# Optimization experiments

Hardware: AMD Instinct MI355X
Metric: run time of the kernel (lower is better)

## Reference

```python
import jax, jax.numpy as jnp
import numpy as np

LORA_R = 32
LORA_ALPHA = 64
SCALING = LORA_ALPHA / LORA_R  # LoraLinear.scaling_
INIT_STD = 0.02  # router_init_range_


def setup_inputs() -> dict:
    key = jax.random.key(0)
    k0, k1, k2, k3, k4 = jax.random.split(key, 5)
    B, S, D, O, E, R = 4, 4096, 3072, 3072, 8, LORA_R
    x = jax.random.normal(k0, (B, S, D), jnp.float32)
    W = jax.random.normal(k1, (O, D), jnp.float32) * INIT_STD          # base_layer weight
    gate_w = jax.random.normal(k2, (E, D), jnp.float32) * INIT_STD     # router gate
    lora_A = jax.random.normal(k3, (E, R, D), jnp.float32) * INIT_STD  # per-expert lora_A.weight
    lora_B = jax.random.normal(k4, (E, O, R), jnp.float32) * INIT_STD  # per-expert lora_B.weight
    return {"x": x, "W": W, "gate_w": gate_w, "lora_A": lora_A, "lora_B": lora_B, "top_k": 2}


def reference(x, W, gate_w, lora_A, lora_B, top_k):
    # MixLoRA routing: softmax gate -> top-k -> renormalize -> per-expert LoRA -> combine.
    B, S, D = x.shape
    E = gate_w.shape[0]
    xt = x.reshape(-1, D)                       # [T, D], T = B*S
    residual = xt @ W.T                         # base_layer(hidden_states)
    logits = xt @ gate_w.T                      # [T, E]
    probs = jax.nn.softmax(logits, axis=-1)
    top_w, top_i = jax.lax.top_k(probs, top_k)  # [T, k]
    top_w = top_w / top_w.sum(-1, keepdims=True)
    # per-token per-expert combine weight (0 for unselected experts) [T, E]
    oh = jax.nn.one_hot(top_i, E, dtype=xt.dtype)          # [T, k, E]
    w_te = jnp.einsum('tke,tk->te', oh, top_w)             # [T, E]
    # dense-dispatch equivalent of gather/scatter: unselected experts have weight 0
    a = jnp.einsum('td,erd->ter', xt, lora_A)              # [T, E, R]  (dropout = identity, eval)
    y = jnp.einsum('ter,eor,te->to', a, lora_B, w_te)      # [T, O]
    out = residual + SCALING * y
    return out.reshape(B, S, -1)
```

## Files before the change

kernel.cpp:

```cpp
#include <hip/hip_runtime.h>
#include <hip/hip_bf16.h>
#include <stdint.h>

typedef unsigned short u16;
typedef __attribute__((ext_vector_type(8))) short short8;
typedef __attribute__((ext_vector_type(4))) float floatx4;

#define T_NUM 16384
#define D_DIM 3072
#define O_DIM 3072
#define E_NUM 8
#define R_DIM 32
#define KA    (E_NUM * R_DIM)

__device__ __forceinline__ float bf2f(u16 u) {
    union { unsigned int i; float f; } v;
    v.i = ((unsigned int)u) << 16;
    return v.f;
}
__device__ __forceinline__ u16 f2bf(float f) {
    union { float f; unsigned int u; } v;
    v.f = f;
    unsigned int r = (v.u + 0x7FFFu + ((v.u >> 16) & 1u)) >> 16;
    return (u16)r;
}

struct f8 { float v[8]; };

template<bool BF>
__device__ __forceinline__ f8 loadf8(const void* p, size_t idx) {
    f8 r;
    if constexpr (BF) {
        short8 s = *(const short8*)((const u16*)p + idx);
#pragma unroll
        for (int j = 0; j < 8; ++j) r.v[j] = bf2f((u16)s[j]);
    } else {
        const float* f = (const float*)p + idx;
        floatx4 a = *(const floatx4*)f;
        floatx4 b = *(const floatx4*)(f + 4);
#pragma unroll
        for (int j = 0; j < 4; ++j) { r.v[j] = a[j]; r.v[4 + j] = b[j]; }
    }
    return r;
}

template<bool BF>
__device__ __forceinline__ short8 load8bf(const void* p, size_t idx) {
    if constexpr (BF) {
        return *(const short8*)((const u16*)p + idx);
    } else {
        const float* f = (const float*)p + idx;
        floatx4 a = *(const floatx4*)f;
        floatx4 b = *(const floatx4*)(f + 4);
        short8 s;
#pragma unroll
        for (int j = 0; j < 4; ++j) { s[j] = (short)f2bf(a[j]); s[4 + j] = (short)f2bf(b[j]); }
        return s;
    }
}

__device__ __forceinline__ void gload16(const u16* g, const short* l) {
    __builtin_amdgcn_global_load_lds(
        (const __attribute__((address_space(1))) void*)g,
        (__attribute__((address_space(3))) void*)l, 16, 0, 0);
}

#define BARR  asm volatile("s_barrier" ::: "memory")
#define LGKM0 asm volatile("s_waitcnt lgkmcnt(0)" ::: "memory")

__global__ void detect_kernel(const u16* __restrict__ x16, int* __restrict__ flag) {
    __shared__ int cnt;
    if (threadIdx.x == 0) cnt = 0;
    __syncthreads();
    int local = 0;
#pragma unroll
    for (int i = 0; i < 32; ++i) {
        u16 u = x16[(size_t)(threadIdx.x * 32 + i) * 2];
        int e = (u >> 7) & 0xFF;
        local += (e < 100 || e > 150) ? 1 : 0;
    }
    atomicAdd(&cnt, local);
    __syncthreads();
    if (threadIdx.x == 0) *flag = (cnt < 2048) ? 1 : 0;
}

__global__ __launch_bounds__(256) void cvt_kernel(
    const float* __restrict__ src, u16* __restrict__ dst, int n8,
    const int* __restrict__ flag, int want)
{
    if (*flag != want) return;
    int idx = blockIdx.x * 256 + threadIdx.x;
    if (idx >= n8) return;
    short8 s = load8bf<false>(src, (size_t)idx * 8);
    *(short8*)(dst + (size_t)idx * 8) = s;
}

template<bool BF>
__global__ __launch_bounds__(256) void routing_kernel(
    const void* __restrict__ x, const void* __restrict__ gate_w,
    float* __restrict__ s_te, u16* __restrict__ xb,
    const int* __restrict__ flag, int want)
{
    if (*flag != want) return;
    int lane = threadIdx.x & 63;
    int wave = threadIdx.x >> 6;
    int t = blockIdx.x * 4 + wave;

    float acc[E_NUM];
#pragma unroll
    for (int e = 0; e < E_NUM; ++e) acc[e] = 0.f;

#pragma unroll
    for (int i = 0; i < 6; ++i) {
        size_t d = (size_t)(i * 64 + lane) * 8;
        f8 xv = loadf8<BF>(x, (size_t)t * D_DIM + d);
        if constexpr (!BF) {
            if (xb) {
                short8 s;
#pragma unroll
                for (int j = 0; j < 8; ++j) s[j] = (short)f2bf(xv.v[j]);
                *(short8*)(xb + (size_t)t * D_DIM + d) = s;
            }
        }
#pragma unroll
        for (int e = 0; e < E_NUM; ++e) {
            f8 gv = loadf8<BF>(gate_w, (size_t)e * D_DIM + d);
#pragma unroll
            for (int j = 0; j < 8; ++j) acc[e] += xv.v[j] * gv.v[j];
        }
    }
#pragma unroll
    for (int e = 0; e < E_NUM; ++e) {
#pragma unroll
        for (int off = 32; off > 0; off >>= 1)
            acc[e] += __shfl_xor(acc[e], off, 64);
    }
    if (lane == 0) {
        int i0 = 0; float l0 = acc[0];
        for (int e = 1; e < E_NUM; ++e) if (acc[e] > l0) { l0 = acc[e]; i0 = e; }
        int i1 = -1; float l1 = -1e30f;
        for (int e = 0; e < E_NUM; ++e) if (e != i0 && acc[e] > l1) { l1 = acc[e]; i1 = e; }
        float w0 = 1.f / (1.f + __expf(l1 - l0));
        float w1 = 1.f - w0;
        float s[E_NUM];
#pragma unroll
        for (int e = 0; e < E_NUM; ++e) s[e] = 0.f;
        s[i0] = 2.f * w0;
        s[i1] = 2.f * w1;
#pragma unroll
        for (int e = 0; e < E_NUM; ++e) s_te[(size_t)t * E_NUM + e] = s[e];
    }
}

template<bool BF>
__global__ __launch_bounds__(256) void pack_b_kernel(
    const void* __restrict__ loraB, u16* __restrict__ Bp,
    const int* __restrict__ flag, int want)
{
    if (*flag != want) return;
    int idx = blockIdx.x * 256 + threadIdx.x;
    int e = idx / O_DIM;
    int o = idx - e * O_DIM;
#pragma unroll
    for (int i = 0; i < 4; ++i) {
        short8 s = load8bf<BF>(loraB, (size_t)idx * R_DIM + i * 8);
        *(short8*)(Bp + (size_t)o * KA + e * R_DIM + i * 8) = s;
    }
}

template<bool BF1, bool OUTBF>
__global__ __launch_bounds__(256) void gemm_kernel(
    const void* __restrict__ A1, int lda1, int kt1,
    const u16* __restrict__ A2, int lda2, int kt2,
    const void* __restrict__ B1, int ldb1,
    const u16* __restrict__ B2, int ldb2,
    void* __restrict__ outv, int ldo,
    const float* __restrict__ s_te, int scale_mode,
    const int* __restrict__ flag, int want)
{
    if (*flag != want) return;
    __shared__ short As[2][128 * 64];
    __shared__ short Bs[2][128 * 64];

    const int tid  = threadIdx.x;
    const int lane = tid & 63;
    const int wave = tid >> 6;
    const int rowA0 = blockIdx.x * 128;
    const int rowB0 = blockIdx.y * 128;

    floatx4 acc[4][4];
#pragma unroll
    for (int mi = 0; mi < 4; ++mi)
#pragma unroll
        for (int ni = 0; ni < 4; ++ni)
            acc[mi][ni] = (floatx4){0.f, 0.f, 0.f, 0.f};

    const int m_base = (wave & 1) * 64;
    const int n_base = (wave >> 1) * 64;
    const int quad = lane >> 4;
    const int r16  = lane & 15;

    int srow[4], scol[4], soff[4];
#pragma unroll
    for (int i = 0; i < 4; ++i) {
        int c = wave * 256 + i * 64 + lane;
        int r = c >> 3, c8 = c & 7;
        srow[i] = r;
        scol[i] = c8 * 8;
        soff[i] = r * 64 + ((c8 ^ (r & 7)) * 8);
    }

    auto LD = [&](int kt, short8 av[4], short8 bv[4]) {
        if (kt < kt1) {
            const int ko = kt * 64;
#pragma unroll
            for (int i = 0; i < 4; ++i) {
                av[i] = load8bf<BF1>(A1, (size_t)(rowA0 + srow[i]) * lda1 + ko + scol[i]);
                bv[i] = load8bf<BF1>(B1, (size_t)(rowB0 + srow[i]) * ldb1 + ko + scol[i]);
            }
        } else {
            const int ko = (kt - kt1) * 64;
#pragma unroll
            for (int i = 0; i < 4; ++i) {
                av[i] = *(const short8*)(A2 + (size_t)(rowA0 + srow[i]) * lda2 + ko + scol[i]);
                bv[i] = *(const short8*)(B2 + (size_t)(rowB0 + srow[i]) * ldb2 + ko + scol[i]);
            }
        }
    };
    auto ST = [&](int buf, const short8 av[4], const short8 bv[4]) {
#pragma unroll
        for (int i = 0; i < 4; ++i) {
            *(short8*)(&As[buf][soff[i]]) = av[i];
            *(short8*)(&Bs[buf][soff[i]]) = bv[i];
        }
    };

    const int ktot = kt1 + kt2;
    short8 pa[4], pb[4];
    LD(0, pa, pb);
    ST(0, pa, pb);
    __syncthreads();
    int cur = 0;

    for (int kt = 0; kt < ktot; ++kt) {
        const bool more = (kt + 1 < ktot);
        if (more) LD(kt + 1, pa, pb);

#pragma unroll
        for (int kk = 0; kk < 64; kk += 32) {
            short8 af[4], bfg[4];
#pragma unroll
            for (int mi = 0; mi < 4; ++mi) {
                const int row = m_base + mi * 16 + r16;
                af[mi] = *(const short8*)(&As[cur][row * 64 + ((kk + quad * 8) ^ ((row & 7) * 8))]);
            }
#pragma unroll
            for (int ni = 0; ni < 4; ++ni) {
                const int row = n_base + ni * 16 + r16;
                bfg[ni] = *(const short8*)(&Bs[cur][row * 64 + ((kk + quad * 8) ^ ((row & 7) * 8))]);
            }
#pragma unroll
            for (int mi = 0; mi < 4; ++mi)
#pragma unroll
                for (int ni = 0; ni < 4; ++ni)
                    acc[mi][ni] = __builtin_amdgcn_mfma_f32_16x16x32_bf16(
                        af[mi], bfg[ni], acc[mi][ni], 0, 0, 0);
        }

        if (more) {
            ST(cur ^ 1, pa, pb);
            __syncthreads();
            cur ^= 1;
        }
    }

#pragma unroll
    for (int mi = 0; mi < 4; ++mi) {
#pragma unroll
        for (int r = 0; r < 4; ++r) {
            int t = rowA0 + m_base + mi * 16 + quad * 4 + r;
#pragma unroll
            for (int ni = 0; ni < 4; ++ni) {
                int o = rowB0 + n_base + ni * 16 + r16;
                float v = acc[mi][ni][r];
                if (scale_mode) v *= s_te[(size_t)t * E_NUM + (o >> 5)];
                if constexpr (OUTBF)
                    ((u16*)outv)[(size_t)t * ldo + o] = f2bf(v);
                else
                    ((float*)outv)[(size_t)t * ldo + o] = v;
            }
        }
    }
}

template<bool OUTBF>
__global__ __launch_bounds__(512, 2) void gemm256_kernel(
    const u16* __restrict__ A1, int lda1, int kt1,
    const u16* __restrict__ A2, int lda2, int kt2,
    const u16* __restrict__ B1, int ldb1,
    const u16* __restrict__ B2, int ldb2,
    void* __restrict__ outv, int ldo,
    const int* __restrict__ flag, int want)
{
    if (*flag != want) return;
    extern __shared__ short smem[];

    const int tid  = threadIdx.x;
    const int lane = tid & 63;
    const int wave = tid >> 6;
    const int wm   = wave >> 2;
    const int wn   = wave & 3;
    const int quad = lane >> 4;
    const int r16  = lane & 15;
    const int rb   = lane >> 3;
    const int swz  = (lane & 7) ^ rb;

    const int lin = blockIdx.y * 64 + blockIdx.x;
    const int sw  = (lin & 7) * 96 + (lin >> 3);
    const int rowA0 = (sw & 63) * 256;
    const int rowB0 = (sw >> 6) * 256;

    floatx4 acc[8][4];
#pragma unroll
    for (int mi = 0; mi < 8; ++mi)
#pragma unroll
        for (int ni = 0; ni < 4; ++ni)
            acc[mi][ni] = (floatx4){0.f, 0.f, 0.f, 0.f};

    const int ktot = kt1 + kt2;

    auto stA = [&](int nb, int q, int ks) {
        const u16* g;
        if (ks < kt1) g = A1 + (size_t)(rowA0 + q * 8 + rb) * lda1 + (size_t)ks * 64 + swz * 8;
        else          g = A2 + (size_t)(rowA0 + q * 8 + rb) * lda2 + (size_t)(ks - kt1) * 64 + swz * 8;
        gload16(g, smem + nb * 16384 + q * 512);
    };
    auto stB = [&](int nb, int q, int ks) {
        const u16* g;
        if (ks < kt1) g = B1 + (size_t)(rowB0 + q * 8 + rb) * ldb1 + (size_t)ks * 64 + swz * 8;
        else          g = B2 + (size_t)(rowB0 + q * 8 + rb) * ldb2 + (size_t)(ks - kt1) * 64 + swz * 8;
        gload16(g, smem + 32768 + nb * 16384 + q * 512);
    };

    stB(0, wave, 0); stB(0, 8 + wave, 0); stB(0, 16 + wave, 0); stB(0, 24 + wave, 0);
    stA(0, wave, 0); stA(0, 8 + wave, 0); stA(0, 16 + wave, 0); stA(0, 24 + wave, 0);
    asm volatile("s_waitcnt vmcnt(0)" ::: "memory");
    BARR;

    int cur = 0;
    short8 bf[4][2];

    for (int kt = 0; kt < ktot; ++kt) {
        const int  ks   = kt + 1;
        const bool more = ks < ktot;
        const int  nb   = cur ^ 1;
        const short* Acur = smem + cur * 16384;
        const short* Bcur = smem + 32768 + cur * 16384;

        auto rdA = [&](int p, short8 af[2][2]) {
#pragma unroll
            for (int m2 = 0; m2 < 2; ++m2) {
                const int rowm = wm * 128 + (2 * p + m2) * 16 + r16;
                const int sx = rowm & 7;
#pragma unroll
                for (int kx = 0; kx < 2; ++kx)
                    af[m2][kx] = *(const short8*)(Acur + rowm * 64 + (((quad + 4 * kx) ^ sx) * 8));
            }
        };
        auto domfma = [&](int p, short8 af[2][2]) {
#pragma unroll
            for (int m2 = 0; m2 < 2; ++m2)
#pragma unroll
                for (int kx = 0; kx < 2; ++kx)
#pragma unroll
                    for (int ni = 0; ni < 4; ++ni)
                        acc[2 * p + m2][ni] = __builtin_amdgcn_mfma_f32_16x16x32_bf16(
                            af[m2][kx], bf[ni][kx], acc[2 * p + m2][ni], 0, 0, 0);
        };

        short8 af[2][2];

        rdA(0, af);
#pragma unroll
        for (int ni = 0; ni < 4; ++ni) {
            const int rown = wn * 64 + ni * 16 + r16;
            const int sx = rown & 7;
#pragma unroll
            for (int kx = 0; kx < 2; ++kx)
                bf[ni][kx] = *(const short8*)(Bcur + rown * 64 + (((quad + 4 * kx) ^ sx) * 8));
        }
        if (more) { stB(nb, wave, ks); stB(nb, 8 + wave, ks); }
        BARR; LGKM0;
        __builtin_amdgcn_s_setprio(1);
        domfma(0, af);
        __builtin_amdgcn_s_setprio(0);
        BARR;

        rdA(1, af);
        if (more) {
            stB(nb, 16 + wave, ks); stB(nb, 24 + wave, ks);
            stA(nb, wave, ks);      stA(nb, 16 + wave, ks);
            asm volatile("s_waitcnt vmcnt(6)" ::: "memory");
        } else {
            asm volatile("s_waitcnt vmcnt(0)" ::: "memory");
        }
        BARR; LGKM0;
        __builtin_amdgcn_s_setprio(1);
        domfma(1, af);
        __builtin_amdgcn_s_setprio(0);
        BARR;

        rdA(2, af);
        if (more) { stA(nb, 8 + wave, ks); stA(nb, 24 + wave, ks); }
        BARR; LGKM0;
        __builtin_amdgcn_s_setprio(1);
        domfma(2, af);
        __builtin_amdgcn_s_setprio(0);
        BARR;

        rdA(3, af);
        if (more) asm volatile("s_waitcnt vmcnt(2)" ::: "memory");
        BARR; LGKM0;
        __builtin_amdgcn_s_setprio(1);
        domfma(3, af);
        __builtin_amdgcn_s_setprio(0);
        BARR;

        cur = nb;
    }

#pragma unroll
    for (int mi = 0; mi < 8; ++mi) {
#pragma unroll
        for (int r = 0; r < 4; ++r) {
            const int t = rowA0 + wm * 128 + mi * 16 + quad * 4 + r;
#pragma unroll
            for (int ni = 0; ni < 4; ++ni) {
                const int o = rowB0 + wn * 64 + ni * 16 + r16;
                float v = acc[mi][ni][r];
                if constexpr (OUTBF)
                    ((u16*)outv)[(size_t)t * ldo + o] = f2bf(v);
                else
                    ((float*)outv)[(size_t)t * ldo + o] = v;
            }
        }
    }
}

extern "C" void kernel_launch(void* const* d_in, const int* in_sizes, int n_in,
                              void* d_out, int out_size, void* d_ws, size_t ws_size,
                              hipStream_t stream)
{
    const void* x      = d_in[0];
    const void* W      = d_in[1];
    const void* gate_w = d_in[2];
    const void* lora_A = d_in[3];
    const void* lora_B = d_in[4];

    int*   flag     = (int*)d_ws;
    float* s_te     = (float*)((char*)d_ws + 1024);
    u16*   a_scaled = (u16*)((char*)d_ws + 1024 + 524288);
    u16*   B_pack   = (u16*)((char*)d_ws + 1024 + 524288 + 8388608);
    const size_t base_sz = 1024 + 524288 + 8388608 + 1572864;

    const size_t x16_sz = (size_t)T_NUM * D_DIM * 2;
    const size_t W16_sz = (size_t)O_DIM * D_DIM * 2;
    const size_t A16_sz = (size_t)KA * D_DIM * 2;
    const bool big = ws_size >= base_sz + x16_sz + W16_sz + A16_sz;
    u16* x16 = big ? (u16*)((char*)d_ws + base_sz) : nullptr;
    u16* W16 = big ? (u16*)((char*)x16 + x16_sz)   : nullptr;
    u16* A16 = big ? (u16*)((char*)W16 + W16_sz)   : nullptr;

    (void)hipFuncSetAttribute((const void*)gemm256_kernel<true>,
                              hipFuncAttributeMaxDynamicSharedMemorySize, 131072);
    (void)hipFuncSetAttribute((const void*)gemm256_kernel<false>,
                              hipFuncAttributeMaxDynamicSharedMemorySize, 131072);

    detect_kernel<<<1, 256, 0, stream>>>((const u16*)x, flag);

    routing_kernel<true ><<<T_NUM / 4, 256, 0, stream>>>(x, gate_w, s_te, nullptr, flag, 1);
    routing_kernel<false><<<T_NUM / 4, 256, 0, stream>>>(x, gate_w, s_te, x16, flag, 0);

    pack_b_kernel<true ><<<(E_NUM * O_DIM) / 256, 256, 0, stream>>>(lora_B, B_pack, flag, 1);
    pack_b_kernel<false><<<(E_NUM * O_DIM) / 256, 256, 0, stream>>>(lora_B, B_pack, flag, 0);

    const dim3 g2(T_NUM / 256, O_DIM / 256);

    gemm_kernel<true, true><<<dim3(T_NUM / 128, KA / 128), 256, 0, stream>>>(
        x, D_DIM, D_DIM / 64, (const u16*)x, D_DIM, 0,
        lora_A, D_DIM, (const u16*)lora_A, D_DIM,
        a_scaled, KA, s_te, 1, flag, 1);
    gemm256_kernel<true><<<g2, 512, 131072, stream>>>(
        (const u16*)x, D_DIM, D_DIM / 64, a_scaled, KA, KA / 64,
        (const u16*)W, D_DIM, B_pack, KA,
        d_out, O_DIM, flag, 1);

    if (big) {
        cvt_kernel<<<(O_DIM * D_DIM / 8 + 255) / 256, 256, 0, stream>>>(
            (const float*)W, W16, O_DIM * D_DIM / 8, flag, 0);
        cvt_kernel<<<(KA * D_DIM / 8 + 255) / 256, 256, 0, stream>>>(
            (const float*)lora_A, A16, KA * D_DIM / 8, flag, 0);

        gemm_kernel<true, true><<<dim3(T_NUM / 128, KA / 128), 256, 0, stream>>>(
            x16, D_DIM, D_DIM / 64, x16, D_DIM, 0,
            A16, D_DIM, A16, D_DIM,
            a_scaled, KA, s_te, 1, flag, 0);
        gemm256_kernel<false><<<g2, 512, 131072, stream>>>(
            x16, D_DIM, D_DIM / 64, a_scaled, KA, KA / 64,
            W16, D_DIM, B_pack, KA,
            d_out, O_DIM, flag, 0);
    } else {
        gemm_kernel<false, true><<<dim3(T_NUM / 128, KA / 128), 256, 0, stream>>>(
            x, D_DIM, D_DIM / 64, (const u16*)x, D_DIM, 0,
            lora_A, D_DIM, (const u16*)lora_A, D_DIM,
            a_scaled, KA, s_te, 1, flag, 0);
        gemm_kernel<false, false><<<dim3(T_NUM / 128, O_DIM / 128), 256, 0, stream>>>(
            x, D_DIM, D_DIM / 64, a_scaled, KA, 4,
            W, D_DIM, B_pack, KA,
            d_out, O_DIM, nullptr, 0, flag, 0);
    }
}
```

Measured before the change: 831.0 us.

## Precompute GEMM load pointers, grouped tile swizzle, widen detect kernel

The main GEMM now precomputes per-thread global source pointers and advances them by a fixed stride, instead of recomputing the row/column address and the A1/A2 selection on every stage. It also precomputes the LDS read offsets once, which removes per-iteration index and XOR arithmetic. The block-to-tile mapping is changed to group 8 M-tiles per N column, aiming for better L2 reuse. The detect kernel now runs 1024 threads doing 8 loads each instead of 256 threads doing 32, reading the same sampled elements with more parallelism.

After: 804.6 us. 3.2% less time.

```diff
diff --git a/kernel.cpp b/kernel.cpp
--- a/kernel.cpp
+++ b/kernel.cpp
@@ -74,8 +74,8 @@
     __syncthreads();
     int local = 0;
 #pragma unroll
-    for (int i = 0; i < 32; ++i) {
-        u16 u = x16[(size_t)(threadIdx.x * 32 + i) * 2];
+    for (int i = 0; i < 8; ++i) {
+        u16 u = x16[(size_t)(threadIdx.x * 8 + i) * 2];
         int e = (u >> 7) & 0xFF;
         local += (e < 100 || e > 150) ? 1 : 0;
     }
@@ -316,9 +316,10 @@
     const int swz  = (lane & 7) ^ rb;
 
     const int lin = blockIdx.y * 64 + blockIdx.x;
-    const int sw  = (lin & 7) * 96 + (lin >> 3);
-    const int rowA0 = (sw & 63) * 256;
-    const int rowB0 = (sw >> 6) * 256;
+    const int xk  = lin & 7;
+    const int j   = lin >> 3;
+    const int rowA0 = (xk * 8 + (j & 7)) * 256;
+    const int rowB0 = (j >> 3) * 256;
 
     floatx4 acc[8][4];
 #pragma unroll
@@ -327,46 +328,60 @@
         for (int ni = 0; ni < 4; ++ni)
             acc[mi][ni] = (floatx4){0.f, 0.f, 0.f, 0.f};
 
-    const int ktot = kt1 + kt2;
-
-    auto stA = [&](int nb, int q, int ks) {
-        const u16* g;
-        if (ks < kt1) g = A1 + (size_t)(rowA0 + q * 8 + rb) * lda1 + (size_t)ks * 64 + swz * 8;
-        else          g = A2 + (size_t)(rowA0 + q * 8 + rb) * lda2 + (size_t)(ks - kt1) * 64 + swz * 8;
-        gload16(g, smem + nb * 16384 + q * 512);
+    const int sx    = r16 & 7;
+    const int q0    = quad ^ sx;
+    const int aoff0 = (wm * 128 + r16) * 128 + q0 * 16;
+    const int aoff1 = (wm * 128 + r16) * 128 + (q0 ^ 4) * 16;
+    const int boff0 = (wn * 64 + r16) * 128 + q0 * 16;
+    const int boff1 = (wn * 64 + r16) * 128 + (q0 ^ 4) * 16;
+
+    const u16 *pA[4], *pB[4];
+    int rA[4], rB[4];
+#pragma unroll
+    for (int i = 0; i < 4; ++i) {
+        rA[i] = rowA0 + (i * 8 + wave) * 8 + rb;
+        rB[i] = rowB0 + (i * 8 + wave) * 8 + rb;
+        pA[i] = A1 + (size_t)rA[i] * lda1 + swz * 8;
+        pB[i] = B1 + (size_t)rB[i] * ldb1 + swz * 8;
+    }
+
+    auto stA = [&](int nb, int i) {
+        gload16(pA[i], smem + nb * 16384 + (i * 8 + wave) * 512);
+        pA[i] += 64;
     };
-    auto stB = [&](int nb, int q, int ks) {
-        const u16* g;
-        if (ks < kt1) g = B1 + (size_t)(rowB0 + q * 8 + rb) * ldb1 + (size_t)ks * 64 + swz * 8;
-        else          g = B2 + (size_t)(rowB0 + q * 8 + rb) * ldb2 + (size_t)(ks - kt1) * 64 + swz * 8;
-        gload16(g, smem + 32768 + nb * 16384 + q * 512);
+    auto stB = [&](int nb, int i) {
+        gload16(pB[i], smem + 32768 + nb * 16384 + (i * 8 + wave) * 512);
+        pB[i] += 64;
     };
 
-    stB(0, wave, 0); stB(0, 8 + wave, 0); stB(0, 16 + wave, 0); stB(0, 24 + wave, 0);
-    stA(0, wave, 0); stA(0, 8 + wave, 0); stA(0, 16 + wave, 0); stA(0, 24 + wave, 0);
+    stB(0, 0); stB(0, 1); stB(0, 2); stB(0, 3);
+    stA(0, 0); stA(0, 1); stA(0, 2); stA(0, 3);
     asm volatile("s_waitcnt vmcnt(0)" ::: "memory");
     BARR;
 
     int cur = 0;
     short8 bf[4][2];
+    const int ktot = kt1 + kt2;
 
     for (int kt = 0; kt < ktot; ++kt) {
         const int  ks   = kt + 1;
         const bool more = ks < ktot;
         const int  nb   = cur ^ 1;
-        const short* Acur = smem + cur * 16384;
-        const short* Bcur = smem + 32768 + cur * 16384;
-
-        auto rdA = [&](int p, short8 af[2][2]) {
-#pragma unroll
-            for (int m2 = 0; m2 < 2; ++m2) {
-                const int rowm = wm * 128 + (2 * p + m2) * 16 + r16;
-                const int sx = rowm & 7;
-#pragma unroll
-                for (int kx = 0; kx < 2; ++kx)
-                    af[m2][kx] = *(const short8*)(Acur + rowm * 64 + (((quad + 4 * kx) ^ sx) * 8));
-            }
-        };
+
+        if (kt2 > 0 && ks == kt1) {
+#pragma unroll
+            for (int i = 0; i < 4; ++i) {
+                pA[i] = A2 + (size_t)rA[i] * lda2 + swz * 8;
+                pB[i] = B2 + (size_t)rB[i] * ldb2 + swz * 8;
+            }
+        }
+
+        const char* sb   = (const char*)smem + cur * 32768;
+        const char* pa0c = sb + aoff0;
+        const char* pa1c = sb + aoff1;
+        const char* pb0c = sb + 65536 + boff0;
+        const char* pb1c = sb + 65536 + boff1;
+
         auto domfma = [&](int p, short8 af[2][2]) {
 #pragma unroll
             for (int m2 = 0; m2 < 2; ++m2)
@@ -380,26 +395,31 @@
 
         short8 af[2][2];
 
-        rdA(0, af);
+#pragma unroll
+        for (int m2 = 0; m2 < 2; ++m2) {
+            af[m2][0] = *(const short8*)(pa0c + m2 * 2048);
+            af[m2][1] = *(const short8*)(pa1c + m2 * 2048);
+        }
 #pragma unroll
         for (int ni = 0; ni < 4; ++ni) {
-            const int rown = wn * 64 + ni * 16 + r16;
-            const int sx = rown & 7;
-#pragma unroll
-            for (int kx = 0; kx < 2; ++kx)
-                bf[ni][kx] = *(const short8*)(Bcur + rown * 64 + (((quad + 4 * kx) ^ sx) * 8));
-        }
-        if (more) { stB(nb, wave, ks); stB(nb, 8 + wave, ks); }
+            bf[ni][0] = *(const short8*)(pb0c + ni * 2048);
+            bf[ni][1] = *(const short8*)(pb1c + ni * 2048);
+        }
+        if (more) { stB(nb, 0); stB(nb, 1); }
         BARR; LGKM0;
         __builtin_amdgcn_s_setprio(1);
         domfma(0, af);
         __builtin_amdgcn_s_setprio(0);
         BARR;
 
-        rdA(1, af);
+#pragma unroll
+        for (int m2 = 0; m2 < 2; ++m2) {
+            af[m2][0] = *(const short8*)(pa0c + (2 + m2) * 2048);
+            af[m2][1] = *(const short8*)(pa1c + (2 + m2) * 2048);
+        }
         if (more) {
-            stB(nb, 16 + wave, ks); stB(nb, 24 + wave, ks);
-            stA(nb, wave, ks);      stA(nb, 16 + wave, ks);
+            stB(nb, 2); stB(nb, 3);
+            stA(nb, 0); stA(nb, 2);
             asm volatile("s_waitcnt vmcnt(6)" ::: "memory");
         } else {
             asm volatile("s_waitcnt vmcnt(0)" ::: "memory");
@@ -410,15 +430,23 @@
         __builtin_amdgcn_s_setprio(0);
         BARR;
 
-        rdA(2, af);
-        if (more) { stA(nb, 8 + wave, ks); stA(nb, 24 + wave, ks); }
+#pragma unroll
+        for (int m2 = 0; m2 < 2; ++m2) {
+            af[m2][0] = *(const short8*)(pa0c + (4 + m2) * 2048);
+            af[m2][1] = *(const short8*)(pa1c + (4 + m2) * 2048);
+        }
+        if (more) { stA(nb, 1); stA(nb, 3); }
         BARR; LGKM0;
         __builtin_amdgcn_s_setprio(1);
         domfma(2, af);
         __builtin_amdgcn_s_setprio(0);
         BARR;
 
-        rdA(3, af);
+#pragma unroll
+        for (int m2 = 0; m2 < 2; ++m2) {
+            af[m2][0] = *(const short8*)(pa0c + (6 + m2) * 2048);
+            af[m2][1] = *(const short8*)(pa1c + (6 + m2) * 2048);
+        }
         if (more) asm volatile("s_waitcnt vmcnt(2)" ::: "memory");
         BARR; LGKM0;
         __builtin_amdgcn_s_setprio(1);
@@ -476,7 +504,7 @@
     (void)hipFuncSetAttribute((const void*)gemm256_kernel<false>,
                               hipFuncAttributeMaxDynamicSharedMemorySize, 131072);
 
-    detect_kernel<<<1, 256, 0, stream>>>((const u16*)x, flag);
+    detect_kernel<<<1, 1024, 0, stream>>>((const u16*)x, flag);
 
     routing_kernel<true ><<<T_NUM / 4, 256, 0, stream>>>(x, gate_w, s_te, nullptr, flag, 1);
     routing_kernel<false><<<T_NUM / 4, 256, 0, stream>>>(x, gate_w, s_te, x16, flag, 0);
```
